# Performance work log

Hardware: AMD Instinct MI355X
Metric: run time of the kernel (lower is better)

Reference implementation:

```python
import jax, jax.numpy as jnp
import numpy as np
import math

N_CELLS = 65536
HIDDEN = 128
IN_DIM = 64
MAX_DEG = 6
BOND_P = 0.5


def _build_graph():
    """2D lattice bond percolation -> padded adjacency [n, MAX_DEG] + signs + mask."""
    rng = np.random.default_rng(0)
    side = int(math.ceil(math.sqrt(N_CELLS)))
    adj = [[] for _ in range(N_CELLS)]
    for i in range(N_CELLS):
        col = i % side
        r = i + 1
        if col + 1 < side and r < N_CELLS and rng.random() < BOND_P:
            adj[i].append(r); adj[r].append(i)
        d = i + side
        if d < N_CELLS and rng.random() < BOND_P:
            adj[i].append(d); adj[d].append(i)
    for i in range(N_CELLS):  # ring fix for isolated nodes
        if not adj[i]:
            r = (i + 1) % N_CELLS
            adj[i].append(r); adj[r].append(i)
    sign_map = {}
    for i in range(N_CELLS):
        for j in adj[i]:
            key = (min(i, j), max(i, j))
            if key not in sign_map:
                sign_map[key] = 1.0 if rng.random() > 0.5 else -1.0
    nbr = np.zeros((N_CELLS, MAX_DEG), np.int32)
    sgn = np.ones((N_CELLS, MAX_DEG), np.float32)
    msk = np.zeros((N_CELLS, MAX_DEG), bool)
    for i in range(N_CELLS):
        for k, j in enumerate(adj[i][:MAX_DEG]):
            nbr[i, k] = j
            msk[i, k] = True
            sgn[i, k] = sign_map[(min(i, j), max(i, j))]
    return nbr, sgn, msk


def setup_inputs() -> dict:
    key = jax.random.key(0)
    ks = jax.random.split(key, 8)
    nbr, sgn, msk = _build_graph()
    n = N_CELLS
    cell_amp = jax.random.uniform(ks[0], (n, HIDDEN)) * 0.5 + 0.5
    cell_phase = jax.random.normal(ks[1], (n, HIDDEN)) * 0.5 \
        + (2.0 * jnp.pi * jnp.arange(n, dtype=jnp.float32) / n)[:, None]
    phase_vel = jax.random.normal(ks[2], (n, HIDDEN)) * 0.05
    return {
        'x': jax.random.normal(ks[3], (1, IN_DIM)),
        'cell_amp': cell_amp.astype(jnp.float32),
        'cell_phase': cell_phase.astype(jnp.float32),
        'phase_vel': phase_vel.astype(jnp.float32),
        'nbr_idx': jnp.asarray(nbr),
        'nbr_sign': jnp.asarray(sgn),
        'nbr_mask': jnp.asarray(msk),
        'W_in': jax.random.normal(ks[4], (HIDDEN, IN_DIM)) * 0.05,
        'b_in': jax.random.normal(ks[5], (HIDDEN,)) * 0.05,
        'W_dec': jax.random.normal(ks[6], (IN_DIM, 2 * HIDDEN)) * 0.05,
        'b_dec': jax.random.normal(ks[7], (IN_DIM,)) * 0.05,
        'step': 1,
    }


def reference(x, cell_amp, cell_phase, phase_vel, nbr_idx, nbr_sign, nbr_mask,
              W_in, b_in, W_dec, b_dec, step):
    n, h = cell_amp.shape
    # complex cell states, then phase-velocity rotation
    states = (cell_amp * jnp.exp(1j * cell_phase)).astype(jnp.complex64)
    states = states * jnp.exp(1j * phase_vel * 0.1)
    ang = jnp.angle(states)                               # [n, h]

    # --- neighbor interference (vectorized gather over padded adjacency) ---
    nbr_states = states[nbr_idx]                          # [n, d, h]
    nbr_ang = ang[nbr_idx]                                # [n, d, h]
    coupling = jnp.cos(ang[:, None, :] - nbr_ang) * nbr_sign[:, :, None]
    contrib = jnp.where(nbr_mask[:, :, None], coupling * nbr_states * 0.1, 0.0)
    interference = contrib.sum(axis=1)                    # [n, h]
    deg = nbr_mask.sum(axis=-1)                           # [n]
    new = 0.7 * states + 0.3 * interference / jnp.maximum(deg, 1)[:, None]
    new = jnp.where((deg > 0)[:, None], new, states)      # 'continue' for isolated nodes

    # --- morphism toward strongest neighbor (argmax over neighbors) ---
    strength = jnp.abs(states).sum(axis=-1)               # [n]
    nstr = jnp.where(nbr_mask, strength[nbr_idx], -jnp.inf)
    best_slot = jnp.argmax(nstr, axis=1)                  # first max, like python max()
    best = jnp.take_along_axis(nbr_idx, best_slot[:, None], axis=1)[:, 0]
    src = states[best]                                    # [n, h]
    morph = jnp.abs(src) * jnp.exp(1j * (jnp.angle(new) - jnp.angle(src)))
    new = jnp.where((deg >= 2)[:, None], new + 0.02 * morph, new)

    # --- global traveling wave ---
    t = step * 0.1
    wave = 0.02 * jnp.sin(t + 2.0 * jnp.pi * jnp.arange(n, dtype=jnp.float32) / n)
    new = new * (1.0 + wave)[:, None]

    # --- input-driven phase perturbation on first 32 cells ---
    sig = x[0] @ W_in.T + b_in                            # [h]
    pp = sig / (jnp.abs(sig).max() + 1e-8) * jnp.pi * 0.1
    idx = jnp.arange(n, dtype=jnp.float32)
    factor = jnp.where(jnp.arange(n) < 32, 0.1 / (1.0 + 0.1 * idx), 0.0)
    new_ang = jnp.angle(new) + pp[None, :] * factor[:, None]
    new = jnp.abs(new) * jnp.exp(1j * new_ang)

    # --- amplitude renormalization per cell ---
    amp = jnp.abs(new)
    amp = amp / (amp.max(axis=-1, keepdims=True) + 1e-8)
    cs = (amp * jnp.exp(1j * jnp.angle(new))).astype(jnp.complex64)

    # --- readout ---
    mean_state = cs.mean(axis=0)                          # [h]
    out_real = jnp.concatenate([mean_state.real, mean_state.imag])[None, :]
    pred = out_real @ W_dec.T + b_dec                     # [1, IN_DIM]
    tension = jnp.var(jnp.abs(cs), ddof=1)                # torch.var (unbiased)
    return pred, tension
```

## Files before the change

### kernel.cpp

```cpp
#include <hip/hip_runtime.h>
#include <math.h>

#define N_CELLS 65536
#define HIDDEN  128
#define IN_DIM  64
#define MAX_DEG 6

#define WPB    4
#define NPB    32
#define NBLK   (N_CELLS/NPB)
#define CHUNK  8

#define INV2PI 0.15915494309189535f

__device__ __forceinline__ void fsincos(float x, float& s, float& c) {
    const float r = x * INV2PI;
    s = __builtin_amdgcn_sinf(r);
    c = __builtin_amdgcn_cosf(r);
}

#define WS_PP    0
#define WS_FLAG  512
#define WS_STR   1024
#define WS_P     (1024 + N_CELLS*4)
#define WS_SA    (WS_P + 256*NBLK*4)
#define WS_SA2   (WS_SA + NBLK*4)
#define WS_MEAN  (WS_SA2 + NBLK*4)

__global__ __launch_bounds__(256) void k_sp(
    const float* __restrict__ amp, float* __restrict__ strength,
    const float* __restrict__ x, const float* __restrict__ W_in,
    const float* __restrict__ b_in, const unsigned char* __restrict__ maskb,
    float* __restrict__ pp, int* __restrict__ flag)
{
    const int tid = threadIdx.x;
    if (blockIdx.x < N_CELLS/4) {
        const int node = blockIdx.x*4 + (tid >> 6);
        const int lane = tid & 63;
        const float2 v = ((const float2*)(amp + (size_t)node*HIDDEN))[lane];
        float s = v.x + v.y;
        #pragma unroll
        for (int off = 32; off > 0; off >>= 1) s += __shfl_xor(s, off);
        if (lane == 0) strength[node] = s;
        return;
    }
    __shared__ float sig[HIDDEN];
    __shared__ float red[HIDDEN];
    __shared__ int fl[256];
    if (tid < HIDDEN) {
        float acc = b_in[tid];
        #pragma unroll 8
        for (int d = 0; d < IN_DIM; ++d) acc = fmaf(W_in[tid*IN_DIM + d], x[d], acc);
        sig[tid] = acc;
        red[tid] = fabsf(acc);
    }
    int v = 0;
    #pragma unroll
    for (int r = 0; r < 4; ++r) v |= (int)maskb[(tid + 256*r)*4 + 1];
    fl[tid] = v;
    __syncthreads();
    for (int s = 64; s > 0; s >>= 1) {
        if (tid < s) red[tid] = fmaxf(red[tid], red[tid + s]);
        __syncthreads();
    }
    for (int s = 128; s > 0; s >>= 1) {
        if (tid < s) fl[tid] |= fl[tid + s];
        __syncthreads();
    }
    if (tid < HIDDEN) pp[tid] = sig[tid] / (red[0] + 1e-8f) * 0.314159265358979f;
    if (tid == 0) *flag = (fl[0] != 0) ? 1 : 0;
}

__global__ __launch_bounds__(256) void k_main2(
    const float* __restrict__ amp, const float* __restrict__ phase,
    const float* __restrict__ vel, const int* __restrict__ nbr_idx,
    const float* __restrict__ nbr_sign, const void* __restrict__ nbr_mask,
    const int* __restrict__ step, const float* __restrict__ pp,
    const int* __restrict__ flagp, const float* __restrict__ strength,
    float* __restrict__ P, float* __restrict__ p_sa, float* __restrict__ p_sa2)
{
    __shared__ int   lwp[NPB][8];
    __shared__ float lsk[NPB][6];
    const int tid  = threadIdx.x;
    const int blk  = blockIdx.x;
    const int node0 = blk * NPB;

    {
        const int flag = *flagp;
        const unsigned char* mb = (const unsigned char*)nbr_mask;
        const int*           mi = (const int*)nbr_mask;
        if (tid < NPB*MAX_DEG) {
            const int n = tid / MAX_DEG, k = tid - n*MAX_DEG;
            const int e = (node0 + n)*MAX_DEG + k;
            const int m = flag ? (mb[e] != 0) : (mi[e] != 0);
            const int j = nbr_idx[e];
            const float sg = nbr_sign[e];
            lwp[n][k] = m ? (j | ((sg < 0.0f) ? (1<<24) : 0) | (1<<25)) : 0;
            lsk[n][k] = m ? strength[j] : -3.0e38f;
        }
    }
    __syncthreads();
    if (tid < NPB) {
        int deg = 0, bs = 0; float bv = -3.0e38f;
        #pragma unroll
        for (int k = 0; k < MAX_DEG; ++k) {
            deg += (lwp[tid][k] >> 25) & 1;
            const float sv = lsk[tid][k];
            if (sv > bv) { bv = sv; bs = k; }
        }
        lwp[tid][6] = deg;
        lwp[tid][7] = lwp[tid][bs] & 0xFFFFF;
    }
    __syncthreads();

    const int wv   = tid >> 6;
    const int lane = tid & 63;
    const float trev = 0.1f * (float)step[0] * INV2PI;
    const float2 ppv = ((const float2*)pp)[lane];
    const unsigned loff = (unsigned)lane * 8u;

    float accre0=0.f, accre1=0.f, accim0=0.f, accim1=0.f, accsa=0.f, accsa2=0.f;

    for (int c = 0; c < CHUNK; ++c) {
        const int nl = wv*CHUNK + c;
        const int i  = node0 + nl;
        const int4 A0 = *(const int4*)&lwp[nl][0];
        const int4 A1 = *(const int4*)&lwp[nl][4];
        const int deg = A1.z, jb = A1.w;

        const unsigned io = (unsigned)i*512u + loff;
        const float2 av = *(const float2*)((const char*)amp   + io);
        const float2 pv = *(const float2*)((const char*)phase + io);
        const float2 vv = *(const float2*)((const char*)vel   + io);
        float s0,c0,s1,c1;
        fsincos(fmaf(0.1f, vv.x, pv.x), s0, c0);
        fsincos(fmaf(0.1f, vv.y, pv.y), s1, c1);
        const float Ri0 = av.x*c0, Ii0 = av.x*s0, Ri1 = av.y*c1, Ii1 = av.y*s1;

        float ir0=0.f, ii0=0.f, ir1=0.f, ii1=0.f;
        const int slots[MAX_DEG] = {A0.x, A0.y, A0.z, A0.w, A1.x, A1.y};
        #pragma unroll
        for (int k = 0; k < MAX_DEG; ++k) {
            const int w = slots[k];
            const unsigned j = (unsigned)(w & 0xFFFFF);
            const float sgnm = (w & (1<<25)) ? ((w & (1<<24)) ? -1.0f : 1.0f) : 0.0f;
            const unsigned jo = j*512u + loff;
            const float2 aj = *(const float2*)((const char*)amp   + jo);
            const float2 pj = *(const float2*)((const char*)phase + jo);
            const float2 vj = *(const float2*)((const char*)vel   + jo);
            float sj0,cj0,sj1,cj1;
            fsincos(fmaf(0.1f, vj.x, pj.x), sj0, cj0);
            fsincos(fmaf(0.1f, vj.y, pj.y), sj1, cj1);
            const float t0 = (c0*cj0 + s0*sj0) * (sgnm * aj.x);
            const float t1 = (c1*cj1 + s1*sj1) * (sgnm * aj.y);
            ir0 = fmaf(t0, cj0, ir0);  ii0 = fmaf(t0, sj0, ii0);
            ir1 = fmaf(t1, cj1, ir1);  ii1 = fmaf(t1, sj1, ii1);
        }

        const float f = 0.03f * __builtin_amdgcn_rcpf((float)deg);
        float nr0 = fmaf(0.7f, Ri0, f*ir0);
        float ni0 = fmaf(0.7f, Ii0, f*ii0);
        float nr1 = fmaf(0.7f, Ri1, f*ir1);
        float ni1 = fmaf(0.7f, Ii1, f*ii1);

        if (deg >= 2) {
            const unsigned bo = (unsigned)jb*512u + loff;
            const float2 ab = *(const float2*)((const char*)amp   + bo);
            const float2 pb = *(const float2*)((const char*)phase + bo);
            const float2 vb = *(const float2*)((const char*)vel   + bo);
            float sb0,cb0,sb1,cb1;
            fsincos(fmaf(0.1f, vb.x, pb.x), sb0, cb0);
            fsincos(fmaf(0.1f, vb.y, pb.y), sb1, cb1);
            const float Rb0 = ab.x*cb0, Ib0 = ab.x*sb0;
            const float Rb1 = ab.y*cb1, Ib1 = ab.y*sb1;
            const float im0 = 0.02f * __builtin_amdgcn_rsqf(nr0*nr0 + ni0*ni0);
            const float im1 = 0.02f * __builtin_amdgcn_rsqf(nr1*nr1 + ni1*ni1);
            const float mr0 = im0*(nr0*Rb0 + ni0*Ib0);
            const float mi0 = im0*(ni0*Rb0 - nr0*Ib0);
            const float mr1 = im1*(nr1*Rb1 + ni1*Ib1);
            const float mi1 = im1*(ni1*Rb1 - nr1*Ib1);
            nr0 += mr0; ni0 += mi0; nr1 += mr1; ni1 += mi1;
        }

        const float wr = fmaf((float)i, 1.52587890625e-5f, trev);
        const float wf = 1.0f + 0.02f * __builtin_amdgcn_sinf(wr);
        nr0 *= wf; ni0 *= wf; nr1 *= wf; ni1 *= wf;

        if (i < 32) {
            const float fac = 0.1f / fmaf(0.1f, (float)i, 1.0f);
            float sp0,cp0,sp1,cp1;
            fsincos(ppv.x*fac, sp0, cp0);
            fsincos(ppv.y*fac, sp1, cp1);
            float tr = nr0*cp0 - ni0*sp0;  ni0 = ni0*cp0 + nr0*sp0;  nr0 = tr;
            tr       = nr1*cp1 - ni1*sp1;  ni1 = ni1*cp1 + nr1*sp1;  nr1 = tr;
        }

        const float m0 = sqrtf(nr0*nr0 + ni0*ni0);
        const float m1 = sqrtf(nr1*nr1 + ni1*ni1);
        float lm = fmaxf(m0, m1);
        #pragma unroll
        for (int off = 32; off > 0; off >>= 1) lm = fmaxf(lm, __shfl_xor(lm, off));
        const float sc = 1.0f / (lm + 1e-8f);
        accre0 += nr0*sc; accim0 += ni0*sc;
        accre1 += nr1*sc; accim1 += ni1*sc;
        const float Aa = m0*sc, Ab = m1*sc;
        accsa  += Aa + Ab;
        accsa2 += Aa*Aa + Ab*Ab;
    }

    __shared__ float4 lred[WPB][64];
    __shared__ float  lsa[WPB], lsa2[WPB];
    lred[wv][lane] = make_float4(accre0, accre1, accim0, accim1);
    float ss = accsa, ss2 = accsa2;
    #pragma unroll
    for (int off = 32; off > 0; off >>= 1) { ss += __shfl_xor(ss, off); ss2 += __shfl_xor(ss2, off); }
    if (lane == 0) { lsa[wv] = ss; lsa2[wv] = ss2; }
    __syncthreads();
    if (tid < 64) {
        const float4 a = lred[0][tid], b = lred[1][tid], c = lred[2][tid], d = lred[3][tid];
        P[(2*tid  )*NBLK + blk]     = a.x + b.x + c.x + d.x;
        P[(2*tid+1)*NBLK + blk]     = a.y + b.y + c.y + d.y;
        P[(128+2*tid)*NBLK + blk]   = a.z + b.z + c.z + d.z;
        P[(129+2*tid)*NBLK + blk]   = a.w + b.w + c.w + d.w;
    }
    if (tid == 0) {
        p_sa [blk] = lsa[0]  + lsa[1]  + lsa[2]  + lsa[3];
        p_sa2[blk] = lsa2[0] + lsa2[1] + lsa2[2] + lsa2[3];
    }
}

__global__ void k_red(const float* __restrict__ P, float* __restrict__ mean)
{
    __shared__ double red[256];
    const int r = blockIdx.x, tid = threadIdx.x;
    double s = 0.0;
    #pragma unroll
    for (int k = 0; k < NBLK/256; ++k) s += (double)P[(size_t)r*NBLK + tid + 256*k];
    red[tid] = s;
    __syncthreads();
    for (int st = 128; st > 0; st >>= 1) { if (tid < st) red[tid] += red[tid + st]; __syncthreads(); }
    if (tid == 0) mean[r] = (float)(red[0] / (double)N_CELLS);
}

__global__ void k_final(const float* __restrict__ mean_in,
                        const float* __restrict__ p_sa, const float* __restrict__ p_sa2,
                        const float* __restrict__ W_dec, const float* __restrict__ b_dec,
                        float* __restrict__ out)
{
    __shared__ float  mean[2*HIDDEN];
    __shared__ double dred[256];
    __shared__ double tots[2];
    const int tid = threadIdx.x;
    mean[tid] = mean_in[tid];
    double sa = 0.0, sa2 = 0.0;
    #pragma unroll
    for (int k = 0; k < NBLK/256; ++k) {
        sa  += (double)p_sa [tid + 256*k];
        sa2 += (double)p_sa2[tid + 256*k];
    }
    dred[tid] = sa;
    __syncthreads();
    for (int s = 128; s > 0; s >>= 1) { if (tid < s) dred[tid] += dred[tid + s]; __syncthreads(); }
    if (tid == 0) tots[0] = dred[0];
    __syncthreads();
    dred[tid] = sa2;
    __syncthreads();
    for (int s = 128; s > 0; s >>= 1) { if (tid < s) dred[tid] += dred[tid + s]; __syncthreads(); }
    if (tid == 0) tots[1] = dred[0];
    __syncthreads();

    if (tid < IN_DIM) {
        float acc = b_dec[tid];
        #pragma unroll 8
        for (int c = 0; c < 2*HIDDEN; ++c) acc = fmaf(mean[c], W_dec[tid*2*HIDDEN + c], acc);
        out[tid] = acc;
    }
    if (tid == 0) {
        const double M = (double)N_CELLS * (double)HIDDEN;
        const double var = (tots[1] - tots[0]*tots[0]/M) / (M - 1.0);
        out[IN_DIM] = (float)var;
    }
}

extern "C" void kernel_launch(void* const* d_in, const int* in_sizes, int n_in,
                              void* d_out, int out_size, void* d_ws, size_t ws_size,
                              hipStream_t stream)
{
    const float* x       = (const float*)d_in[0];
    const float* amp     = (const float*)d_in[1];
    const float* phase   = (const float*)d_in[2];
    const float* vel     = (const float*)d_in[3];
    const int*   nbr_idx = (const int*)d_in[4];
    const float* nbr_sgn = (const float*)d_in[5];
    const void*  nbr_msk = d_in[6];
    const float* W_in    = (const float*)d_in[7];
    const float* b_in    = (const float*)d_in[8];
    const float* W_dec   = (const float*)d_in[9];
    const float* b_dec   = (const float*)d_in[10];
    const int*   step    = (const int*)d_in[11];

    char* wsb = (char*)d_ws;
    float* pp    = (float*)(wsb + WS_PP);
    int*   flag  = (int*)  (wsb + WS_FLAG);
    float* strg  = (float*)(wsb + WS_STR);
    float* P     = (float*)(wsb + WS_P);
    float* p_sa  = (float*)(wsb + WS_SA);
    float* p_sa2 = (float*)(wsb + WS_SA2);
    float* meanb = (float*)(wsb + WS_MEAN);
    float* out   = (float*)d_out;

    k_sp<<<N_CELLS/4 + 1, 256, 0, stream>>>(amp, strg, x, W_in, b_in,
                                            (const unsigned char*)nbr_msk, pp, flag);
    k_main2<<<NBLK, 256, 0, stream>>>(amp, phase, vel, nbr_idx, nbr_sgn, nbr_msk,
                                      step, pp, flag, strg, P, p_sa, p_sa2);
    k_red<<<256, 256, 0, stream>>>(P, meanb);
    k_final<<<1, 256, 0, stream>>>(meanb, p_sa, p_sa2, W_dec, b_dec, out);
}
```

Before: 78.94 us.

## Precompute per-cell complex state in fp16 and gather neighbors from it

A prepass now computes each cell's rotated complex state (amp·cos, amp·sin) once, stores it as packed half2, and writes the strength sums in the same pass. The main kernel then gathers 16 bytes per lane from this compact buffer for self, neighbors and the morph target, instead of reading three fp32 arrays and redoing sincos for every neighbor. Each half-wave now handles a node with 4 hidden elements per lane, valid neighbors are compacted so the loop can exit early, and the cos/sin terms are recovered by normalizing with rsq. The cost is an extra 32 MB intermediate write plus fp16 precision loss, and the neighbor index mask is narrowed from 20 to 16 bits.

```diff
diff --git a/kernel.cpp b/kernel.cpp
--- a/kernel.cpp
+++ b/kernel.cpp
@@ -1,4 +1,5 @@
 #include <hip/hip_runtime.h>
+#include <hip/hip_fp16.h>
 #include <math.h>
 
 #define N_CELLS 65536
@@ -9,7 +10,7 @@
 #define WPB    4
 #define NPB    32
 #define NBLK   (N_CELLS/NPB)
-#define CHUNK  8
+#define CHUNK  4
 
 #define INV2PI 0.15915494309189535f
 
@@ -22,26 +23,43 @@
 #define WS_PP    0
 #define WS_FLAG  512
 #define WS_STR   1024
-#define WS_P     (1024 + N_CELLS*4)
+#define WS_S     (1024 + N_CELLS*4)
+#define WS_P     (WS_S + (size_t)N_CELLS*512)
 #define WS_SA    (WS_P + 256*NBLK*4)
 #define WS_SA2   (WS_SA + NBLK*4)
 #define WS_MEAN  (WS_SA2 + NBLK*4)
 
-__global__ __launch_bounds__(256) void k_sp(
-    const float* __restrict__ amp, float* __restrict__ strength,
+__global__ __launch_bounds__(256) void k_pre(
+    const float* __restrict__ amp, const float* __restrict__ phase,
+    const float* __restrict__ vel,
     const float* __restrict__ x, const float* __restrict__ W_in,
     const float* __restrict__ b_in, const unsigned char* __restrict__ maskb,
+    int4* __restrict__ S, float* __restrict__ strength,
     float* __restrict__ pp, int* __restrict__ flag)
 {
     const int tid = threadIdx.x;
-    if (blockIdx.x < N_CELLS/4) {
-        const int node = blockIdx.x*4 + (tid >> 6);
-        const int lane = tid & 63;
-        const float2 v = ((const float2*)(amp + (size_t)node*HIDDEN))[lane];
-        float s = v.x + v.y;
-        #pragma unroll
-        for (int off = 32; off > 0; off >>= 1) s += __shfl_xor(s, off);
-        if (lane == 0) strength[node] = s;
+    if (blockIdx.x < N_CELLS/8) {
+        const int node = blockIdx.x*8 + (tid >> 5);
+        const int hl   = tid & 31;
+        const size_t ro = (size_t)node*HIDDEN + 4*hl;
+        const float4 a = *(const float4*)(amp   + ro);
+        const float4 p = *(const float4*)(phase + ro);
+        const float4 v = *(const float4*)(vel   + ro);
+        float s0,c0,s1,c1,s2,c2,s3,c3;
+        fsincos(fmaf(0.1f, v.x, p.x), s0, c0);
+        fsincos(fmaf(0.1f, v.y, p.y), s1, c1);
+        fsincos(fmaf(0.1f, v.z, p.z), s2, c2);
+        fsincos(fmaf(0.1f, v.w, p.w), s3, c3);
+        union { int4 v4; __half2 h[4]; } u;
+        u.h[0] = __floats2half2_rn(a.x*c0, a.x*s0);
+        u.h[1] = __floats2half2_rn(a.y*c1, a.y*s1);
+        u.h[2] = __floats2half2_rn(a.z*c2, a.z*s2);
+        u.h[3] = __floats2half2_rn(a.w*c3, a.w*s3);
+        S[(size_t)node*32 + hl] = u.v4;
+        float st = a.x + a.y + a.z + a.w;
+        #pragma unroll
+        for (int off = 16; off > 0; off >>= 1) st += __shfl_xor(st, off);
+        if (hl == 0) strength[node] = st;
         return;
     }
     __shared__ float sig[HIDDEN];
@@ -71,157 +89,188 @@
     if (tid == 0) *flag = (fl[0] != 0) ? 1 : 0;
 }
 
-__global__ __launch_bounds__(256) void k_main2(
-    const float* __restrict__ amp, const float* __restrict__ phase,
-    const float* __restrict__ vel, const int* __restrict__ nbr_idx,
+__global__ __launch_bounds__(256) void k_mainc(
+    const int4* __restrict__ S, const int* __restrict__ nbr_idx,
     const float* __restrict__ nbr_sign, const void* __restrict__ nbr_mask,
     const int* __restrict__ step, const float* __restrict__ pp,
     const int* __restrict__ flagp, const float* __restrict__ strength,
     float* __restrict__ P, float* __restrict__ p_sa, float* __restrict__ p_sa2)
 {
+    __shared__ int   lji[NPB][MAX_DEG];
+    __shared__ float lsk[NPB][MAX_DEG];
     __shared__ int   lwp[NPB][8];
-    __shared__ float lsk[NPB][6];
-    const int tid  = threadIdx.x;
-    const int blk  = blockIdx.x;
+    __shared__ float4 lredre[WPB][32], lredim[WPB][32];
+    __shared__ float  lsa[WPB], lsa2[WPB];
+
+    const int tid   = threadIdx.x;
+    const int blk   = blockIdx.x;
     const int node0 = blk * NPB;
 
-    {
-        const int flag = *flagp;
+    if (tid < NPB*MAX_DEG) {
+        const int flagv = *flagp;
         const unsigned char* mb = (const unsigned char*)nbr_mask;
         const int*           mi = (const int*)nbr_mask;
-        if (tid < NPB*MAX_DEG) {
-            const int n = tid / MAX_DEG, k = tid - n*MAX_DEG;
-            const int e = (node0 + n)*MAX_DEG + k;
-            const int m = flag ? (mb[e] != 0) : (mi[e] != 0);
-            const int j = nbr_idx[e];
-            const float sg = nbr_sign[e];
-            lwp[n][k] = m ? (j | ((sg < 0.0f) ? (1<<24) : 0) | (1<<25)) : 0;
-            lsk[n][k] = m ? strength[j] : -3.0e38f;
-        }
+        const int n = tid / MAX_DEG, k = tid - n*MAX_DEG;
+        const int e = (node0 + n)*MAX_DEG + k;
+        const int m = flagv ? (mb[e] != 0) : (mi[e] != 0);
+        const int j = nbr_idx[e];
+        const float sg = nbr_sign[e];
+        lji[n][k] = m ? (j | ((sg < 0.0f) ? (1<<24) : 0) | (1<<25)) : 0;
+        lsk[n][k] = m ? strength[j] : -3.0e38f;
     }
     __syncthreads();
     if (tid < NPB) {
-        int deg = 0, bs = 0; float bv = -3.0e38f;
+        int cnt = 0, jb = 0; float bv = -3.0e38f;
         #pragma unroll
         for (int k = 0; k < MAX_DEG; ++k) {
-            deg += (lwp[tid][k] >> 25) & 1;
+            const int w = lji[tid][k];
+            if (w >> 25) lwp[tid][cnt++] = w;
             const float sv = lsk[tid][k];
-            if (sv > bv) { bv = sv; bs = k; }
-        }
-        lwp[tid][6] = deg;
-        lwp[tid][7] = lwp[tid][bs] & 0xFFFFF;
+            if (sv > bv) { bv = sv; jb = w & 0xFFFF; }
+        }
+        for (int k = cnt; k < MAX_DEG; ++k) lwp[tid][k] = 0;
+        lwp[tid][6] = cnt;
+        lwp[tid][7] = jb;
     }
     __syncthreads();
 
     const int wv   = tid >> 6;
     const int lane = tid & 63;
+    const int half = lane >> 5;
+    const int lh   = lane & 31;
     const float trev = 0.1f * (float)step[0] * INV2PI;
-    const float2 ppv = ((const float2*)pp)[lane];
-    const unsigned loff = (unsigned)lane * 8u;
-
-    float accre0=0.f, accre1=0.f, accim0=0.f, accim1=0.f, accsa=0.f, accsa2=0.f;
+    const float4 ppv = ((const float4*)pp)[lh];
+
+    float accre[4] = {0,0,0,0}, accim[4] = {0,0,0,0};
+    float accsa = 0.f, accsa2 = 0.f;
 
     for (int c = 0; c < CHUNK; ++c) {
-        const int nl = wv*CHUNK + c;
+        const int nl = wv*(2*CHUNK) + 2*c + half;
         const int i  = node0 + nl;
         const int4 A0 = *(const int4*)&lwp[nl][0];
         const int4 A1 = *(const int4*)&lwp[nl][4];
         const int deg = A1.z, jb = A1.w;
-
-        const unsigned io = (unsigned)i*512u + loff;
-        const float2 av = *(const float2*)((const char*)amp   + io);
-        const float2 pv = *(const float2*)((const char*)phase + io);
-        const float2 vv = *(const float2*)((const char*)vel   + io);
-        float s0,c0,s1,c1;
-        fsincos(fmaf(0.1f, vv.x, pv.x), s0, c0);
-        fsincos(fmaf(0.1f, vv.y, pv.y), s1, c1);
-        const float Ri0 = av.x*c0, Ii0 = av.x*s0, Ri1 = av.y*c1, Ii1 = av.y*s1;
-
-        float ir0=0.f, ii0=0.f, ir1=0.f, ii1=0.f;
+        const int kmax = max(deg, __shfl_xor(deg, 32));
+
+        union { int4 v4; __half2 h[4]; } us;
+        us.v4 = S[(size_t)i*32 + lh];
+        float R[4], I[4], inva[4];
+        #pragma unroll
+        for (int q = 0; q < 4; ++q) {
+            const float2 e = __half22float2(us.h[q]);
+            R[q] = e.x; I[q] = e.y;
+            inva[q] = __builtin_amdgcn_rsqf(e.x*e.x + e.y*e.y);
+        }
+
+        float ir[4] = {0,0,0,0}, ii[4] = {0,0,0,0};
         const int slots[MAX_DEG] = {A0.x, A0.y, A0.z, A0.w, A1.x, A1.y};
         #pragma unroll
         for (int k = 0; k < MAX_DEG; ++k) {
+            if (k >= kmax) break;
             const int w = slots[k];
-            const unsigned j = (unsigned)(w & 0xFFFFF);
+            const unsigned j = (unsigned)(w & 0xFFFF);
             const float sgnm = (w & (1<<25)) ? ((w & (1<<24)) ? -1.0f : 1.0f) : 0.0f;
-            const unsigned jo = j*512u + loff;
-            const float2 aj = *(const float2*)((const char*)amp   + jo);
-            const float2 pj = *(const float2*)((const char*)phase + jo);
-            const float2 vj = *(const float2*)((const char*)vel   + jo);
-            float sj0,cj0,sj1,cj1;
-            fsincos(fmaf(0.1f, vj.x, pj.x), sj0, cj0);
-            fsincos(fmaf(0.1f, vj.y, pj.y), sj1, cj1);
-            const float t0 = (c0*cj0 + s0*sj0) * (sgnm * aj.x);
-            const float t1 = (c1*cj1 + s1*sj1) * (sgnm * aj.y);
-            ir0 = fmaf(t0, cj0, ir0);  ii0 = fmaf(t0, sj0, ii0);
-            ir1 = fmaf(t1, cj1, ir1);  ii1 = fmaf(t1, sj1, ii1);
+            union { int4 v4; __half2 h[4]; } uj;
+            uj.v4 = S[(size_t)j*32 + lh];
+            #pragma unroll
+            for (int q = 0; q < 4; ++q) {
+                const float2 e = __half22float2(uj.h[q]);
+                const float E = R[q]*e.x + I[q]*e.y;
+                const float g = sgnm * E * __builtin_amdgcn_rsqf(e.x*e.x + e.y*e.y);
+                ir[q] = fmaf(g, e.x, ir[q]);
+                ii[q] = fmaf(g, e.y, ii[q]);
+            }
         }
 
         const float f = 0.03f * __builtin_amdgcn_rcpf((float)deg);
-        float nr0 = fmaf(0.7f, Ri0, f*ir0);
-        float ni0 = fmaf(0.7f, Ii0, f*ii0);
-        float nr1 = fmaf(0.7f, Ri1, f*ir1);
-        float ni1 = fmaf(0.7f, Ii1, f*ii1);
+        float nr[4], ni[4];
+        #pragma unroll
+        for (int q = 0; q < 4; ++q) {
+            const float fq = f * inva[q];
+            nr[q] = fmaf(0.7f, R[q], fq*ir[q]);
+            ni[q] = fmaf(0.7f, I[q], fq*ii[q]);
+        }
 
         if (deg >= 2) {
-            const unsigned bo = (unsigned)jb*512u + loff;
-            const float2 ab = *(const float2*)((const char*)amp   + bo);
-            const float2 pb = *(const float2*)((const char*)phase + bo);
-            const float2 vb = *(const float2*)((const char*)vel   + bo);
-            float sb0,cb0,sb1,cb1;
-            fsincos(fmaf(0.1f, vb.x, pb.x), sb0, cb0);
-            fsincos(fmaf(0.1f, vb.y, pb.y), sb1, cb1);
-            const float Rb0 = ab.x*cb0, Ib0 = ab.x*sb0;
-            const float Rb1 = ab.y*cb1, Ib1 = ab.y*sb1;
-            const float im0 = 0.02f * __builtin_amdgcn_rsqf(nr0*nr0 + ni0*ni0);
-            const float im1 = 0.02f * __builtin_amdgcn_rsqf(nr1*nr1 + ni1*ni1);
-            const float mr0 = im0*(nr0*Rb0 + ni0*Ib0);
-            const float mi0 = im0*(ni0*Rb0 - nr0*Ib0);
-            const float mr1 = im1*(nr1*Rb1 + ni1*Ib1);
-            const float mi1 = im1*(ni1*Rb1 - nr1*Ib1);
-            nr0 += mr0; ni0 += mi0; nr1 += mr1; ni1 += mi1;
+            union { int4 v4; __half2 h[4]; } ub;
+            ub.v4 = S[(size_t)jb*32 + lh];
+            #pragma unroll
+            for (int q = 0; q < 4; ++q) {
+                const float2 e = __half22float2(ub.h[q]);
+                const float im = 0.02f * __builtin_amdgcn_rsqf(nr[q]*nr[q] + ni[q]*ni[q]);
+                const float mr = im*(nr[q]*e.x + ni[q]*e.y);
+                const float mi = im*(ni[q]*e.x - nr[q]*e.y);
+                nr[q] += mr; ni[q] += mi;
+            }
         }
 
         const float wr = fmaf((float)i, 1.52587890625e-5f, trev);
         const float wf = 1.0f + 0.02f * __builtin_amdgcn_sinf(wr);
-        nr0 *= wf; ni0 *= wf; nr1 *= wf; ni1 *= wf;
+        #pragma unroll
+        for (int q = 0; q < 4; ++q) { nr[q] *= wf; ni[q] *= wf; }
 
         if (i < 32) {
             const float fac = 0.1f / fmaf(0.1f, (float)i, 1.0f);
-            float sp0,cp0,sp1,cp1;
-            fsincos(ppv.x*fac, sp0, cp0);
-            fsincos(ppv.y*fac, sp1, cp1);
-            float tr = nr0*cp0 - ni0*sp0;  ni0 = ni0*cp0 + nr0*sp0;  nr0 = tr;
-            tr       = nr1*cp1 - ni1*sp1;  ni1 = ni1*cp1 + nr1*sp1;  nr1 = tr;
-        }
-
-        const float m0 = sqrtf(nr0*nr0 + ni0*ni0);
-        const float m1 = sqrtf(nr1*nr1 + ni1*ni1);
-        float lm = fmaxf(m0, m1);
-        #pragma unroll
-        for (int off = 32; off > 0; off >>= 1) lm = fmaxf(lm, __shfl_xor(lm, off));
+            const float pv[4] = {ppv.x, ppv.y, ppv.z, ppv.w};
+            #pragma unroll
+            for (int q = 0; q < 4; ++q) {
+                float sp, cp;
+                fsincos(pv[q]*fac, sp, cp);
+                const float tr = nr[q]*cp - ni[q]*sp;
+                ni[q] = ni[q]*cp + nr[q]*sp;
+                nr[q] = tr;
+            }
+        }
+
+        float m[4];
+        #pragma unroll
+        for (int q = 0; q < 4; ++q) m[q] = sqrtf(nr[q]*nr[q] + ni[q]*ni[q]);
+        float lm = fmaxf(fmaxf(m[0], m[1]), fmaxf(m[2], m[3]));
+        #pragma unroll
+        for (int off = 16; off > 0; off >>= 1) lm = fmaxf(lm, __shfl_xor(lm, off));
         const float sc = 1.0f / (lm + 1e-8f);
-        accre0 += nr0*sc; accim0 += ni0*sc;
-        accre1 += nr1*sc; accim1 += ni1*sc;
-        const float Aa = m0*sc, Ab = m1*sc;
-        accsa  += Aa + Ab;
-        accsa2 += Aa*Aa + Ab*Ab;
-    }
-
-    __shared__ float4 lred[WPB][64];
-    __shared__ float  lsa[WPB], lsa2[WPB];
-    lred[wv][lane] = make_float4(accre0, accre1, accim0, accim1);
-    float ss = accsa, ss2 = accsa2;
-    #pragma unroll
-    for (int off = 32; off > 0; off >>= 1) { ss += __shfl_xor(ss, off); ss2 += __shfl_xor(ss2, off); }
-    if (lane == 0) { lsa[wv] = ss; lsa2[wv] = ss2; }
-    __syncthreads();
-    if (tid < 64) {
-        const float4 a = lred[0][tid], b = lred[1][tid], c = lred[2][tid], d = lred[3][tid];
-        P[(2*tid  )*NBLK + blk]     = a.x + b.x + c.x + d.x;
-        P[(2*tid+1)*NBLK + blk]     = a.y + b.y + c.y + d.y;
-        P[(128+2*tid)*NBLK + blk]   = a.z + b.z + c.z + d.z;
-        P[(129+2*tid)*NBLK + blk]   = a.w + b.w + c.w + d.w;
+        #pragma unroll
+        for (int q = 0; q < 4; ++q) {
+            accre[q] += nr[q]*sc;
+            accim[q] += ni[q]*sc;
+            const float A = m[q]*sc;
+            accsa  += A;
+            accsa2 += A*A;
+        }
+    }
+
+    #pragma unroll
+    for (int q = 0; q < 4; ++q) {
+        accre[q] += __shfl_xor(accre[q], 32);
+        accim[q] += __shfl_xor(accim[q], 32);
+    }
+    #pragma unroll
+    for (int off = 32; off > 0; off >>= 1) {
+        accsa  += __shfl_xor(accsa,  off);
+        accsa2 += __shfl_xor(accsa2, off);
+    }
+    if (half == 0) {
+        lredre[wv][lh] = make_float4(accre[0], accre[1], accre[2], accre[3]);
+        lredim[wv][lh] = make_float4(accim[0], accim[1], accim[2], accim[3]);
+    }
+    if (lane == 0) { lsa[wv] = accsa; lsa2[wv] = accsa2; }
+    __syncthreads();
+    if (tid < 32) {
+        float4 r = lredre[0][tid], im = lredim[0][tid];
+        #pragma unroll
+        for (int w = 1; w < WPB; ++w) {
+            const float4 a = lredre[w][tid], b = lredim[w][tid];
+            r.x += a.x; r.y += a.y; r.z += a.z; r.w += a.w;
+            im.x += b.x; im.y += b.y; im.z += b.z; im.w += b.w;
+        }
+        P[(4*tid  )*NBLK + blk]       = r.x;
+        P[(4*tid+1)*NBLK + blk]       = r.y;
+        P[(4*tid+2)*NBLK + blk]       = r.z;
+        P[(4*tid+3)*NBLK + blk]       = r.w;
+        P[(128+4*tid  )*NBLK + blk]   = im.x;
+        P[(128+4*tid+1)*NBLK + blk]   = im.y;
+        P[(128+4*tid+2)*NBLK + blk]   = im.z;
+        P[(128+4*tid+3)*NBLK + blk]   = im.w;
     }
     if (tid == 0) {
         p_sa [blk] = lsa[0]  + lsa[1]  + lsa[2]  + lsa[3];
@@ -303,15 +352,17 @@
     float* pp    = (float*)(wsb + WS_PP);
     int*   flag  = (int*)  (wsb + WS_FLAG);
     float* strg  = (float*)(wsb + WS_STR);
+    int4*  S     = (int4*) (wsb + WS_S);
     float* P     = (float*)(wsb + WS_P);
     float* p_sa  = (float*)(wsb + WS_SA);
     float* p_sa2 = (float*)(wsb + WS_SA2);
     float* meanb = (float*)(wsb + WS_MEAN);
     float* out   = (float*)d_out;
 
-    k_sp<<<N_CELLS/4 + 1, 256, 0, stream>>>(amp, strg, x, W_in, b_in,
-                                            (const unsigned char*)nbr_msk, pp, flag);
-    k_main2<<<NBLK, 256, 0, stream>>>(amp, phase, vel, nbr_idx, nbr_sgn, nbr_msk,
+    k_pre<<<N_CELLS/8 + 1, 256, 0, stream>>>(amp, phase, vel, x, W_in, b_in,
+                                             (const unsigned char*)nbr_msk,
+                                             S, strg, pp, flag);
+    k_mainc<<<NBLK, 256, 0, stream>>>(S, nbr_idx, nbr_sgn, nbr_msk,
                                       step, pp, flag, strg, P, p_sa, p_sa2);
     k_red<<<256, 256, 0, stream>>>(P, meanb);
     k_final<<<1, 256, 0, stream>>>(meanb, p_sa, p_sa2, W_dec, b_dec, out);
```

After: 70.41 us. 1.12x faster.
